# Kernel optimization log

Measured on AMD Instinct MI355X. Metric: run time of the kernel, lower is better.

The kernel has to match this reference:

```python
import jax, jax.numpy as jnp
import numpy as np
from functools import partial

T = 2048        # num tokens
H = 2048        # hidden_size
I = 1024        # intermediate_size (per TP rank)
E = 8           # num_local_experts
TOP_K = 2       # num_experts_per_tok


def setup_inputs() -> dict:
    key = jax.random.key(0)
    k1, k2, k3, k4 = jax.random.split(key, 4)
    hidden_states = jax.random.normal(k1, (T, H), dtype=jnp.float32)
    gate_w = jax.random.normal(k2, (E, H), dtype=jnp.float32) * (H ** -0.5)
    # ws: [E, 2I, H] merged w1(gate)+w3(up); w2s: [E, H, I]
    ws = jax.random.normal(k3, (E, 2 * I, H), dtype=jnp.float32) * (H ** -0.5)
    w2s = jax.random.normal(k4, (E, H, I), dtype=jnp.float32) * (I ** -0.5)
    return {"hidden_states": hidden_states, "gate_w": gate_w, "ws": ws, "w2s": w2s}


def _moe_forward(x, gate_w, ws, w2s):
    num_tokens = x.shape[0]
    # router: replicated linear -> softmax -> top-k (fused_topk semantics)
    router_logits = x @ gate_w.T                     # [T, E]
    probs = jax.nn.softmax(router_logits, axis=-1)
    topk_weights, topk_ids = jax.lax.top_k(probs, TOP_K)   # [T, K]
    if TOP_K > 1:  # renormalize (do_normalize = top_k > 1)
        topk_weights = topk_weights / jnp.sum(topk_weights, axis=-1, keepdims=True)
    # combine weights as dense [T, E] (zero where expert not selected)
    cw = jnp.zeros((num_tokens, E), dtype=x.dtype)
    cw = cw.at[jnp.arange(num_tokens)[:, None], topk_ids].add(topk_weights)
    # grouped expert GEMMs; loop over the small fixed expert set
    out = jnp.zeros_like(x)
    for e in range(E):
        gate_up = x @ ws[e].T                        # [T, 2I]
        act = jax.nn.silu(gate_up[:, :I]) * gate_up[:, I:]  # SiluAndMul
        out = out + cw[:, e:e + 1] * (act @ w2s[e].T)       # [T, H]
    return out


def reference(hidden_states, gate_w, ws, w2s):
    return _moe_forward(hidden_states, gate_w, ws, w2s)
```

## Files before the change

### kernel.cpp

```cpp
#include <hip/hip_runtime.h>
#include <hip/hip_bf16.h>
#include <stdint.h>

#define TOKS  2048
#define HID   2048
#define ITR   1024
#define NEXP  8
#define NROWS 4096

typedef __attribute__((ext_vector_type(4))) float f32x4;
typedef __attribute__((ext_vector_type(8))) __bf16 bf16x8;
typedef __attribute__((ext_vector_type(8))) unsigned short u16x8;
typedef __attribute__((ext_vector_type(4))) unsigned short u16x4;

__device__ __forceinline__ unsigned short f2bf(float f) {
    union { float f; uint32_t u; } c; c.f = f;
    return (unsigned short)((c.u + 0x7FFFu + ((c.u >> 16) & 1u)) >> 16);
}

__device__ __forceinline__ void gll16(const unsigned short* g, unsigned short* l) {
    __builtin_amdgcn_global_load_lds(
        (const __attribute__((address_space(1))) unsigned int*)g,
        (__attribute__((address_space(3))) unsigned int*)l,
        16, 0, 0);
}

__global__ __launch_bounds__(256) void prep_kernel(const float* __restrict__ ws,
                                                   const float* __restrict__ w2s,
                                                   float* __restrict__ out,
                                                   unsigned short* __restrict__ da,
                                                   unsigned short* __restrict__ db) {
    const int NA = (NEXP * 2 * ITR * HID) / 8;
    const int NB = (NEXP * HID * ITR) / 8;
    const int NO = (TOKS * HID) / 8;
    const int i0 = blockIdx.x * 256 + threadIdx.x;
    const int stride = gridDim.x * 256;
    for (int k = i0; k < NA; k += stride) {
        const f32x4* p = (const f32x4*)(ws + (size_t)k * 8);
        f32x4 a = p[0], b = p[1];
        u16x8 o;
#pragma unroll
        for (int j = 0; j < 4; ++j) { o[j] = f2bf(a[j]); o[4 + j] = f2bf(b[j]); }
        *(u16x8*)(da + (size_t)k * 8) = o;
    }
    for (int k = i0; k < NB; k += stride) {
        const f32x4* p = (const f32x4*)(w2s + (size_t)k * 8);
        f32x4 a = p[0], b = p[1];
        u16x8 o;
#pragma unroll
        for (int j = 0; j < 4; ++j) { o[j] = f2bf(a[j]); o[4 + j] = f2bf(b[j]); }
        *(u16x8*)(db + (size_t)k * 8) = o;
    }
    const f32x4 z = (f32x4){0.f, 0.f, 0.f, 0.f};
    for (int k = i0; k < NO; k += stride) {
        f32x4* q = (f32x4*)(out + (size_t)k * 8);
        q[0] = z; q[1] = z;
    }
}

__global__ __launch_bounds__(64) void router_kernel(const float* __restrict__ x,
                                                    const float* __restrict__ gw,
                                                    unsigned short* __restrict__ xb,
                                                    int* __restrict__ topk_id,
                                                    float* __restrict__ topk_w) {
    const int t = blockIdx.x;
    const int lane = threadIdx.x;
    float acc[NEXP];
#pragma unroll
    for (int e = 0; e < NEXP; ++e) acc[e] = 0.f;
    const float* xr = x + (size_t)t * HID;
    unsigned short* xbr = xb + (size_t)t * HID;
    for (int s4 = lane; s4 < HID / 4; s4 += 64) {
        const f32x4 xv = *(const f32x4*)(xr + s4 * 4);
        u16x4 o;
#pragma unroll
        for (int j = 0; j < 4; ++j) o[j] = f2bf(xv[j]);
        *(u16x4*)(xbr + s4 * 4) = o;
#pragma unroll
        for (int e = 0; e < NEXP; ++e) {
            const f32x4 gv = *(const f32x4*)(gw + e * HID + s4 * 4);
            acc[e] += xv[0] * gv[0] + xv[1] * gv[1] + xv[2] * gv[2] + xv[3] * gv[3];
        }
    }
#pragma unroll
    for (int e = 0; e < NEXP; ++e) {
        float v = acc[e];
        for (int off = 32; off > 0; off >>= 1) v += __shfl_down(v, off, 64);
        acc[e] = v;
    }
    if (lane == 0) {
        float m0 = -1e30f, m1 = -1e30f; int i0 = 0, i1 = 0;
#pragma unroll
        for (int e = 0; e < NEXP; ++e) {
            float v = acc[e];
            if (v > m0) { m1 = m0; i1 = i0; m0 = v; i0 = e; }
            else if (v > m1) { m1 = v; i1 = e; }
        }
        float w0 = 1.f / (1.f + expf(m1 - m0));
        float w1 = 1.f - w0;
        topk_id[t * 2] = i0; topk_id[t * 2 + 1] = i1;
        topk_w[t * 2] = w0;  topk_w[t * 2 + 1] = w1;
    }
}

__global__ __launch_bounds__(512) void sort_kernel(const int* __restrict__ topk_id,
                                                   const float* __restrict__ topk_w,
                                                   int* __restrict__ sorted_tok,
                                                   float* __restrict__ row_w,
                                                   int* __restrict__ offsets,
                                                   int* __restrict__ counts) {
    __shared__ int sc[512 * NEXP];
    __shared__ int base[NEXP + 1];
    const int t = threadIdx.x;
    int ids[8];
    int* myrow = &sc[t * NEXP];
#pragma unroll
    for (int e = 0; e < NEXP; ++e) myrow[e] = 0;
#pragma unroll
    for (int j = 0; j < 8; ++j) { ids[j] = topk_id[t * 8 + j]; myrow[ids[j]]++; }
    __syncthreads();
    for (int d = 1; d < 512; d <<= 1) {
        int add[NEXP];
        const bool act = (t >= d);
#pragma unroll
        for (int e = 0; e < NEXP; ++e) add[e] = act ? sc[(t - d) * NEXP + e] : 0;
        __syncthreads();
        if (act) {
#pragma unroll
            for (int e = 0; e < NEXP; ++e) sc[t * NEXP + e] += add[e];
        }
        __syncthreads();
    }
    if (t == 0) {
        int s = 0;
        for (int e = 0; e < NEXP; ++e) {
            const int tot = sc[511 * NEXP + e];
            base[e] = s; offsets[e] = s; counts[e] = tot; s += tot;
        }
        base[NEXP] = s; offsets[NEXP] = s;
    }
    __syncthreads();
    int own[NEXP];
#pragma unroll
    for (int e = 0; e < NEXP; ++e) {
        int c = 0;
#pragma unroll
        for (int j = 0; j < 8; ++j) c += (ids[j] == e) ? 1 : 0;
        own[e] = c;
    }
#pragma unroll
    for (int e = 0; e < NEXP; ++e) myrow[e] = base[e] + myrow[e] - own[e];
#pragma unroll
    for (int j = 0; j < 8; ++j) {
        const int p = t * 8 + j;
        const int pos = myrow[ids[j]]++;
        sorted_tok[pos] = p >> 1;
        row_w[pos] = topk_w[p];
    }
}

__global__ __launch_bounds__(512) void gemm1_kernel(const unsigned short* __restrict__ Wb,
                                                    const unsigned short* __restrict__ Xb,
                                                    const int* __restrict__ offsets,
                                                    const int* __restrict__ counts,
                                                    const int* __restrict__ sorted_tok,
                                                    unsigned short* __restrict__ act) {
    const int b = blockIdx.x;
    const int e = b & 7;
    const int r = b >> 3;
    const int mt = r >> 4;
    const int nt = r & 15;
    const int cnt = counts[e];
    if (mt * 128 >= cnt) return;
    const int offs = offsets[e];
    const int tid = threadIdx.x, lane = tid & 63, wid = tid >> 6;
    const int wr = wid >> 2, wc = wid & 3;

    __shared__ unsigned short sA[3][128 * 32];
    __shared__ unsigned short sB[3][128 * 32];

    const int srow = tid >> 2;
    const int swz = (((tid & 3) ^ (srow & 3))) * 8;
    int ar = mt * 128 + srow;
    if (ar >= cnt) ar = cnt - 1;
    const int tok = sorted_tok[offs + ar];
    const unsigned short* aSrc = Xb + (size_t)tok * HID + swz;
    const unsigned short* wBase = Wb + (size_t)e * (2 * ITR) * HID;
    const int wrow = (srow < 64) ? (nt * 64 + srow) : (ITR + nt * 64 + (srow - 64));
    const unsigned short* bSrc = wBase + (size_t)wrow * HID + swz;
    const int ldsOff = wid * 16 * 32;

    f32x4 accg[4], accu[4];
#pragma unroll
    for (int i = 0; i < 4; ++i) {
        accg[i] = (f32x4){0.f, 0.f, 0.f, 0.f};
        accu[i] = (f32x4){0.f, 0.f, 0.f, 0.f};
    }

#define G1_STAGE(ks) do {                                  \
        const int k0_ = (ks) * 32;                         \
        gll16(aSrc + k0_, sA[(ks) % 3] + ldsOff);          \
        gll16(bSrc + k0_, sB[(ks) % 3] + ldsOff);          \
    } while (0)

    G1_STAGE(0);
    G1_STAGE(1);

    const int fr = lane & 15, fq = lane >> 4;
    const int sfo = (fq ^ (fr & 3)) * 8;
    const int NS = HID / 32;
    for (int ks = 0; ks < NS; ++ks) {
        const int cur = ks % 3;
        if (ks == NS - 1) asm volatile("s_waitcnt vmcnt(0)" ::: "memory");
        else              asm volatile("s_waitcnt vmcnt(2)" ::: "memory");
        __builtin_amdgcn_s_barrier();
        asm volatile("" ::: "memory");
        if (ks + 2 < NS) G1_STAGE(ks + 2);
        bf16x8 af[4], bg, bu;
#pragma unroll
        for (int mi = 0; mi < 4; ++mi)
            af[mi] = *(const bf16x8*)&sA[cur][(wr * 64 + mi * 16 + fr) * 32 + sfo];
        bg = *(const bf16x8*)&sB[cur][(wc * 16 + fr) * 32 + sfo];
        bu = *(const bf16x8*)&sB[cur][(64 + wc * 16 + fr) * 32 + sfo];
        __builtin_amdgcn_s_setprio(1);
#pragma unroll
        for (int mi = 0; mi < 4; ++mi) {
            accg[mi] = __builtin_amdgcn_mfma_f32_16x16x32_bf16(af[mi], bg, accg[mi], 0, 0, 0);
            accu[mi] = __builtin_amdgcn_mfma_f32_16x16x32_bf16(af[mi], bu, accu[mi], 0, 0, 0);
        }
        __builtin_amdgcn_s_setprio(0);
        asm volatile("" ::: "memory");
    }
#undef G1_STAGE

#pragma unroll
    for (int mi = 0; mi < 4; ++mi) {
#pragma unroll
        for (int j = 0; j < 4; ++j) {
            const int gr = mt * 128 + wr * 64 + mi * 16 + fq * 4 + j;
            if (gr < cnt) {
                const float g = accg[mi][j], u = accu[mi][j];
                const float s = g / (1.f + expf(-g));
                act[(size_t)(offs + gr) * ITR + nt * 64 + wc * 16 + fr] = f2bf(s * u);
            }
        }
    }
}

__global__ __launch_bounds__(512) void gemm2_kernel(const unsigned short* __restrict__ W2b,
                                                    const unsigned short* __restrict__ actb,
                                                    const int* __restrict__ offsets,
                                                    const int* __restrict__ counts,
                                                    const int* __restrict__ sorted_tok,
                                                    const float* __restrict__ row_w,
                                                    float* __restrict__ out) {
    const int b = blockIdx.x;
    const int e = b & 7;
    const int r = b >> 3;
    const int mt = r >> 4;
    const int nt = r & 15;
    const int cnt = counts[e];
    if (mt * 128 >= cnt) return;
    const int offs = offsets[e];
    const int tid = threadIdx.x, lane = tid & 63, wid = tid >> 6;
    const int wr = wid >> 2, wc = wid & 3;

    __shared__ unsigned short sA[3][128 * 32];
    __shared__ unsigned short sB[3][128 * 32];

    const int srow = tid >> 2;
    const int swz = (((tid & 3) ^ (srow & 3))) * 8;
    int ar = mt * 128 + srow;
    if (ar >= cnt) ar = cnt - 1;
    const unsigned short* aSrc = actb + (size_t)(offs + ar) * ITR + swz;
    const unsigned short* bSrc = W2b + ((size_t)e * HID + nt * 128 + srow) * ITR + swz;
    const int ldsOff = wid * 16 * 32;

    f32x4 acc[4][2];
#pragma unroll
    for (int i = 0; i < 4; ++i)
#pragma unroll
        for (int j = 0; j < 2; ++j) acc[i][j] = (f32x4){0.f, 0.f, 0.f, 0.f};

#define G2_STAGE(ks) do {                                  \
        const int k0_ = (ks) * 32;                         \
        gll16(aSrc + k0_, sA[(ks) % 3] + ldsOff);          \
        gll16(bSrc + k0_, sB[(ks) % 3] + ldsOff);          \
    } while (0)

    G2_STAGE(0);
    G2_STAGE(1);

    const int fr = lane & 15, fq = lane >> 4;
    const int sfo = (fq ^ (fr & 3)) * 8;
    const int NS = ITR / 32;
    for (int ks = 0; ks < NS; ++ks) {
        const int cur = ks % 3;
        if (ks == NS - 1) asm volatile("s_waitcnt vmcnt(0)" ::: "memory");
        else              asm volatile("s_waitcnt vmcnt(2)" ::: "memory");
        __builtin_amdgcn_s_barrier();
        asm volatile("" ::: "memory");
        if (ks + 2 < NS) G2_STAGE(ks + 2);
        bf16x8 af[4], bfv[2];
#pragma unroll
        for (int mi = 0; mi < 4; ++mi)
            af[mi] = *(const bf16x8*)&sA[cur][(wr * 64 + mi * 16 + fr) * 32 + sfo];
#pragma unroll
        for (int ni = 0; ni < 2; ++ni)
            bfv[ni] = *(const bf16x8*)&sB[cur][(wc * 32 + ni * 16 + fr) * 32 + sfo];
        __builtin_amdgcn_s_setprio(1);
#pragma unroll
        for (int mi = 0; mi < 4; ++mi)
#pragma unroll
            for (int ni = 0; ni < 2; ++ni)
                acc[mi][ni] = __builtin_amdgcn_mfma_f32_16x16x32_bf16(af[mi], bfv[ni], acc[mi][ni], 0, 0, 0);
        __builtin_amdgcn_s_setprio(0);
        asm volatile("" ::: "memory");
    }
#undef G2_STAGE

#pragma unroll
    for (int mi = 0; mi < 4; ++mi) {
#pragma unroll
        for (int j = 0; j < 4; ++j) {
            const int gr = mt * 128 + wr * 64 + mi * 16 + fq * 4 + j;
            if (gr < cnt) {
                const int pos = offs + gr;
                const int t = sorted_tok[pos];
                const float w = row_w[pos];
#pragma unroll
                for (int ni = 0; ni < 2; ++ni) {
                    const int col = nt * 128 + wc * 32 + ni * 16 + fr;
                    atomicAdd(&out[(size_t)t * HID + col], w * acc[mi][ni][j]);
                }
            }
        }
    }
}

extern "C" void kernel_launch(void* const* d_in, const int* in_sizes, int n_in,
                              void* d_out, int out_size, void* d_ws, size_t ws_size,
                              hipStream_t stream) {
    const float* x   = (const float*)d_in[0];
    const float* gw  = (const float*)d_in[1];
    const float* ws  = (const float*)d_in[2];
    const float* w2s = (const float*)d_in[3];
    float* out = (float*)d_out;

    char* wsb = (char*)d_ws;
    int*   counts     = (int*)(wsb + 0);
    int*   offsets    = (int*)(wsb + 256);
    int*   topk_id    = (int*)(wsb + 4096);
    float* topk_w     = (float*)(wsb + 20480);
    int*   sorted_tok = (int*)(wsb + 36864);
    float* row_w      = (float*)(wsb + 53248);
    unsigned short* xb    = (unsigned short*)(wsb + (1u << 20));
    unsigned short* actb  = (unsigned short*)(wsb + 9437184);
    unsigned short* wsb16 = (unsigned short*)(wsb + 17825792);
    unsigned short* w2b   = (unsigned short*)(wsb + 84934656);

    prep_kernel<<<2048, 256, 0, stream>>>(ws, w2s, out, wsb16, w2b);
    router_kernel<<<TOKS, 64, 0, stream>>>(x, gw, xb, topk_id, topk_w);
    sort_kernel<<<1, 512, 0, stream>>>(topk_id, topk_w, sorted_tok, row_w, offsets, counts);
    gemm1_kernel<<<2048, 512, 0, stream>>>(wsb16, xb, offsets, counts, sorted_tok, actb);
    gemm2_kernel<<<2048, 512, 0, stream>>>(w2b, actb, offsets, counts, sorted_tok, row_w, out);
}
```

Measured before the change: 174.9 us.

## Fuse router into prep kernel, widen conversion loads, reorder GEMM tile indexing

The router computation moves into the weight-conversion prep kernel, run by the first wave of each of the 2048 blocks, which removes one kernel launch. The fp32-to-bf16 conversion and output zeroing now process 16 elements per thread iteration instead of 8. Both GEMMs swap the mt/nt decode of the block index so that consecutive blocks of an expert walk M tiles within a fixed N tile, which changes weight-tile reuse in cache and the ordering of early-exit blocks. The router work adds imbalance to one wave per prep block, but prep is dominated by converting about 200MB of weights.

```diff
diff --git a/kernel.cpp b/kernel.cpp
--- a/kernel.cpp
+++ b/kernel.cpp
@@ -27,79 +27,87 @@
 
 __global__ __launch_bounds__(256) void prep_kernel(const float* __restrict__ ws,
                                                    const float* __restrict__ w2s,
+                                                   const float* __restrict__ x,
+                                                   const float* __restrict__ gw,
                                                    float* __restrict__ out,
                                                    unsigned short* __restrict__ da,
-                                                   unsigned short* __restrict__ db) {
-    const int NA = (NEXP * 2 * ITR * HID) / 8;
-    const int NB = (NEXP * HID * ITR) / 8;
-    const int NO = (TOKS * HID) / 8;
-    const int i0 = blockIdx.x * 256 + threadIdx.x;
+                                                   unsigned short* __restrict__ db,
+                                                   unsigned short* __restrict__ xb,
+                                                   int* __restrict__ topk_id,
+                                                   float* __restrict__ topk_w) {
+    const int tid = threadIdx.x;
+
+    if (tid < 64) {
+        const int t = blockIdx.x;
+        const int lane = tid;
+        float acc[NEXP];
+#pragma unroll
+        for (int e = 0; e < NEXP; ++e) acc[e] = 0.f;
+        const float* xr = x + (size_t)t * HID;
+        unsigned short* xbr = xb + (size_t)t * HID;
+        for (int s4 = lane; s4 < HID / 4; s4 += 64) {
+            const f32x4 xv = *(const f32x4*)(xr + s4 * 4);
+            u16x4 o;
+#pragma unroll
+            for (int j = 0; j < 4; ++j) o[j] = f2bf(xv[j]);
+            *(u16x4*)(xbr + s4 * 4) = o;
+#pragma unroll
+            for (int e = 0; e < NEXP; ++e) {
+                const f32x4 gv = *(const f32x4*)(gw + e * HID + s4 * 4);
+                acc[e] += xv[0] * gv[0] + xv[1] * gv[1] + xv[2] * gv[2] + xv[3] * gv[3];
+            }
+        }
+#pragma unroll
+        for (int e = 0; e < NEXP; ++e) {
+            float v = acc[e];
+            for (int off = 32; off > 0; off >>= 1) v += __shfl_down(v, off, 64);
+            acc[e] = v;
+        }
+        if (lane == 0) {
+            float m0 = -1e30f, m1 = -1e30f; int i0 = 0, i1 = 0;
+#pragma unroll
+            for (int e = 0; e < NEXP; ++e) {
+                float v = acc[e];
+                if (v > m0) { m1 = m0; i1 = i0; m0 = v; i0 = e; }
+                else if (v > m1) { m1 = v; i1 = e; }
+            }
+            float w0 = 1.f / (1.f + expf(m1 - m0));
+            topk_id[t * 2] = i0; topk_id[t * 2 + 1] = i1;
+            topk_w[t * 2] = w0;  topk_w[t * 2 + 1] = 1.f - w0;
+        }
+    }
+
+    const int NA = (NEXP * 2 * ITR * HID) / 16;
+    const int NB = (NEXP * HID * ITR) / 16;
+    const int NO = (TOKS * HID) / 16;
+    const int i0 = blockIdx.x * 256 + tid;
     const int stride = gridDim.x * 256;
     for (int k = i0; k < NA; k += stride) {
-        const f32x4* p = (const f32x4*)(ws + (size_t)k * 8);
-        f32x4 a = p[0], b = p[1];
-        u16x8 o;
-#pragma unroll
-        for (int j = 0; j < 4; ++j) { o[j] = f2bf(a[j]); o[4 + j] = f2bf(b[j]); }
-        *(u16x8*)(da + (size_t)k * 8) = o;
+        const f32x4* p = (const f32x4*)(ws + (size_t)k * 16);
+        f32x4 a = p[0], b = p[1], c = p[2], d = p[3];
+        u16x8 o0, o1;
+#pragma unroll
+        for (int j = 0; j < 4; ++j) { o0[j] = f2bf(a[j]); o0[4 + j] = f2bf(b[j]); }
+#pragma unroll
+        for (int j = 0; j < 4; ++j) { o1[j] = f2bf(c[j]); o1[4 + j] = f2bf(d[j]); }
+        *(u16x8*)(da + (size_t)k * 16) = o0;
+        *(u16x8*)(da + (size_t)k * 16 + 8) = o1;
     }
     for (int k = i0; k < NB; k += stride) {
-        const f32x4* p = (const f32x4*)(w2s + (size_t)k * 8);
-        f32x4 a = p[0], b = p[1];
-        u16x8 o;
-#pragma unroll
-        for (int j = 0; j < 4; ++j) { o[j] = f2bf(a[j]); o[4 + j] = f2bf(b[j]); }
-        *(u16x8*)(db + (size_t)k * 8) = o;
+        const f32x4* p = (const f32x4*)(w2s + (size_t)k * 16);
+        f32x4 a = p[0], b = p[1], c = p[2], d = p[3];
+        u16x8 o0, o1;
+#pragma unroll
+        for (int j = 0; j < 4; ++j) { o0[j] = f2bf(a[j]); o0[4 + j] = f2bf(b[j]); }
+#pragma unroll
+        for (int j = 0; j < 4; ++j) { o1[j] = f2bf(c[j]); o1[4 + j] = f2bf(d[j]); }
+        *(u16x8*)(db + (size_t)k * 16) = o0;
+        *(u16x8*)(db + (size_t)k * 16 + 8) = o1;
     }
     const f32x4 z = (f32x4){0.f, 0.f, 0.f, 0.f};
     for (int k = i0; k < NO; k += stride) {
-        f32x4* q = (f32x4*)(out + (size_t)k * 8);
-        q[0] = z; q[1] = z;
-    }
-}
-
-__global__ __launch_bounds__(64) void router_kernel(const float* __restrict__ x,
-                                                    const float* __restrict__ gw,
-                                                    unsigned short* __restrict__ xb,
-                                                    int* __restrict__ topk_id,
-                                                    float* __restrict__ topk_w) {
-    const int t = blockIdx.x;
-    const int lane = threadIdx.x;
-    float acc[NEXP];
-#pragma unroll
-    for (int e = 0; e < NEXP; ++e) acc[e] = 0.f;
-    const float* xr = x + (size_t)t * HID;
-    unsigned short* xbr = xb + (size_t)t * HID;
-    for (int s4 = lane; s4 < HID / 4; s4 += 64) {
-        const f32x4 xv = *(const f32x4*)(xr + s4 * 4);
-        u16x4 o;
-#pragma unroll
-        for (int j = 0; j < 4; ++j) o[j] = f2bf(xv[j]);
-        *(u16x4*)(xbr + s4 * 4) = o;
-#pragma unroll
-        for (int e = 0; e < NEXP; ++e) {
-            const f32x4 gv = *(const f32x4*)(gw + e * HID + s4 * 4);
-            acc[e] += xv[0] * gv[0] + xv[1] * gv[1] + xv[2] * gv[2] + xv[3] * gv[3];
-        }
-    }
-#pragma unroll
-    for (int e = 0; e < NEXP; ++e) {
-        float v = acc[e];
-        for (int off = 32; off > 0; off >>= 1) v += __shfl_down(v, off, 64);
-        acc[e] = v;
-    }
-    if (lane == 0) {
-        float m0 = -1e30f, m1 = -1e30f; int i0 = 0, i1 = 0;
-#pragma unroll
-        for (int e = 0; e < NEXP; ++e) {
-            float v = acc[e];
-            if (v > m0) { m1 = m0; i1 = i0; m0 = v; i0 = e; }
-            else if (v > m1) { m1 = v; i1 = e; }
-        }
-        float w0 = 1.f / (1.f + expf(m1 - m0));
-        float w1 = 1.f - w0;
-        topk_id[t * 2] = i0; topk_id[t * 2 + 1] = i1;
-        topk_w[t * 2] = w0;  topk_w[t * 2 + 1] = w1;
+        f32x4* q = (f32x4*)(out + (size_t)k * 16);
+        q[0] = z; q[1] = z; q[2] = z; q[3] = z;
     }
 }
 
@@ -168,8 +176,8 @@
     const int b = blockIdx.x;
     const int e = b & 7;
     const int r = b >> 3;
-    const int mt = r >> 4;
-    const int nt = r & 15;
+    const int nt = r >> 4;
+    const int mt = r & 15;
     const int cnt = counts[e];
     if (mt * 128 >= cnt) return;
     const int offs = offsets[e];
@@ -257,8 +265,8 @@
     const int b = blockIdx.x;
     const int e = b & 7;
     const int r = b >> 3;
-    const int mt = r >> 4;
-    const int nt = r & 15;
+    const int nt = r >> 4;
+    const int mt = r & 15;
     const int cnt = counts[e];
     if (mt * 128 >= cnt) return;
     const int offs = offsets[e];
@@ -359,8 +367,7 @@
     unsigned short* wsb16 = (unsigned short*)(wsb + 17825792);
     unsigned short* w2b   = (unsigned short*)(wsb + 84934656);
 
-    prep_kernel<<<2048, 256, 0, stream>>>(ws, w2s, out, wsb16, w2b);
-    router_kernel<<<TOKS, 64, 0, stream>>>(x, gw, xb, topk_id, topk_w);
+    prep_kernel<<<2048, 256, 0, stream>>>(ws, w2s, x, gw, out, wsb16, w2b, xb, topk_id, topk_w);
     sort_kernel<<<1, 512, 0, stream>>>(topk_id, topk_w, sorted_tok, row_w, offsets, counts);
     gemm1_kernel<<<2048, 512, 0, stream>>>(wsb16, xb, offsets, counts, sorted_tok, actb);
     gemm2_kernel<<<2048, 512, 0, stream>>>(w2b, actb, offsets, counts, sorted_tok, row_w, out);
```

Measured after the change: 234.6 us. +34.2%, slower.

## Fuse fp32-to-bf16 weight conversion into GEMM loads, drop prep kernel

Applied to the files above, without the earlier changes.

Removes the separate prep pass that converted all expert weights to bf16 and zeroed the output. The GEMM kernels now stream fp32 weights straight into LDS via global_load_lds and convert to bf16 in registers before each MFMA, and the output is zeroed with hipMemsetAsync. This saves one full read-and-write pass over the weights. In exchange, B-tile global traffic and LDS footprint double, each stage issues an extra load, and per-iteration conversion ALU work is added. Weight tiles are also re-read from global memory by every M-tile block rather than once.

```diff
diff --git a/kernel.cpp b/kernel.cpp
--- a/kernel.cpp
+++ b/kernel.cpp
@@ -18,44 +18,11 @@
     return (unsigned short)((c.u + 0x7FFFu + ((c.u >> 16) & 1u)) >> 16);
 }
 
-__device__ __forceinline__ void gll16(const unsigned short* g, unsigned short* l) {
+__device__ __forceinline__ void gll16(const void* g, void* l) {
     __builtin_amdgcn_global_load_lds(
         (const __attribute__((address_space(1))) unsigned int*)g,
         (__attribute__((address_space(3))) unsigned int*)l,
         16, 0, 0);
-}
-
-__global__ __launch_bounds__(256) void prep_kernel(const float* __restrict__ ws,
-                                                   const float* __restrict__ w2s,
-                                                   float* __restrict__ out,
-                                                   unsigned short* __restrict__ da,
-                                                   unsigned short* __restrict__ db) {
-    const int NA = (NEXP * 2 * ITR * HID) / 8;
-    const int NB = (NEXP * HID * ITR) / 8;
-    const int NO = (TOKS * HID) / 8;
-    const int i0 = blockIdx.x * 256 + threadIdx.x;
-    const int stride = gridDim.x * 256;
-    for (int k = i0; k < NA; k += stride) {
-        const f32x4* p = (const f32x4*)(ws + (size_t)k * 8);
-        f32x4 a = p[0], b = p[1];
-        u16x8 o;
-#pragma unroll
-        for (int j = 0; j < 4; ++j) { o[j] = f2bf(a[j]); o[4 + j] = f2bf(b[j]); }
-        *(u16x8*)(da + (size_t)k * 8) = o;
-    }
-    for (int k = i0; k < NB; k += stride) {
-        const f32x4* p = (const f32x4*)(w2s + (size_t)k * 8);
-        f32x4 a = p[0], b = p[1];
-        u16x8 o;
-#pragma unroll
-        for (int j = 0; j < 4; ++j) { o[j] = f2bf(a[j]); o[4 + j] = f2bf(b[j]); }
-        *(u16x8*)(db + (size_t)k * 8) = o;
-    }
-    const f32x4 z = (f32x4){0.f, 0.f, 0.f, 0.f};
-    for (int k = i0; k < NO; k += stride) {
-        f32x4* q = (f32x4*)(out + (size_t)k * 8);
-        q[0] = z; q[1] = z;
-    }
 }
 
 __global__ __launch_bounds__(64) void router_kernel(const float* __restrict__ x,
@@ -97,9 +64,8 @@
             else if (v > m1) { m1 = v; i1 = e; }
         }
         float w0 = 1.f / (1.f + expf(m1 - m0));
-        float w1 = 1.f - w0;
         topk_id[t * 2] = i0; topk_id[t * 2 + 1] = i1;
-        topk_w[t * 2] = w0;  topk_w[t * 2 + 1] = w1;
+        topk_w[t * 2] = w0;  topk_w[t * 2 + 1] = 1.f - w0;
     }
 }
 
@@ -159,7 +125,7 @@
     }
 }
 
-__global__ __launch_bounds__(512) void gemm1_kernel(const unsigned short* __restrict__ Wb,
+__global__ __launch_bounds__(512) void gemm1_kernel(const float* __restrict__ W,
                                                     const unsigned short* __restrict__ Xb,
                                                     const int* __restrict__ offsets,
                                                     const int* __restrict__ counts,
@@ -177,7 +143,7 @@
     const int wr = wid >> 2, wc = wid & 3;
 
     __shared__ unsigned short sA[3][128 * 32];
-    __shared__ unsigned short sB[3][128 * 32];
+    __shared__ float sBf[3][128 * 32];
 
     const int srow = tid >> 2;
     const int swz = (((tid & 3) ^ (srow & 3))) * 8;
@@ -185,10 +151,19 @@
     if (ar >= cnt) ar = cnt - 1;
     const int tok = sorted_tok[offs + ar];
     const unsigned short* aSrc = Xb + (size_t)tok * HID + swz;
-    const unsigned short* wBase = Wb + (size_t)e * (2 * ITR) * HID;
-    const int wrow = (srow < 64) ? (nt * 64 + srow) : (ITR + nt * 64 + (srow - 64));
-    const unsigned short* bSrc = wBase + (size_t)wrow * HID + swz;
-    const int ldsOff = wid * 16 * 32;
+    const int ldsA = wid * 16 * 32;
+
+    const int l8 = lane & 7;
+    const int rr = lane >> 3;
+    const int foff = (((l8 >> 1) ^ (rr & 3)) * 8) + (l8 & 1) * 4;
+    const int R1 = wid * 16 + rr;
+    const int R2 = R1 + 8;
+    const int g1row = (R1 < 64) ? (nt * 64 + R1) : (ITR + nt * 64 + (R1 - 64));
+    const int g2row = (R2 < 64) ? (nt * 64 + R2) : (ITR + nt * 64 + (R2 - 64));
+    const float* bSrc1 = W + ((size_t)e * 2 * ITR + g1row) * HID + foff;
+    const float* bSrc2 = W + ((size_t)e * 2 * ITR + g2row) * HID + foff;
+    const int ldsB1 = (wid * 16) * 32;
+    const int ldsB2 = (wid * 16 + 8) * 32;
 
     f32x4 accg[4], accu[4];
 #pragma unroll
@@ -199,8 +174,9 @@
 
 #define G1_STAGE(ks) do {                                  \
         const int k0_ = (ks) * 32;                         \
-        gll16(aSrc + k0_, sA[(ks) % 3] + ldsOff);          \
-        gll16(bSrc + k0_, sB[(ks) % 3] + ldsOff);          \
+        gll16(aSrc + k0_, sA[(ks) % 3] + ldsA);            \
+        gll16(bSrc1 + k0_, sBf[(ks) % 3] + ldsB1);         \
+        gll16(bSrc2 + k0_, sBf[(ks) % 3] + ldsB2);         \
     } while (0)
 
     G1_STAGE(0);
@@ -208,20 +184,29 @@
 
     const int fr = lane & 15, fq = lane >> 4;
     const int sfo = (fq ^ (fr & 3)) * 8;
+    const int slot32 = fq ^ (fr & 3);
     const int NS = HID / 32;
     for (int ks = 0; ks < NS; ++ks) {
         const int cur = ks % 3;
         if (ks == NS - 1) asm volatile("s_waitcnt vmcnt(0)" ::: "memory");
-        else              asm volatile("s_waitcnt vmcnt(2)" ::: "memory");
+        else              asm volatile("s_waitcnt vmcnt(3)" ::: "memory");
         __builtin_amdgcn_s_barrier();
         asm volatile("" ::: "memory");
         if (ks + 2 < NS) G1_STAGE(ks + 2);
-        bf16x8 af[4], bg, bu;
+        bf16x8 af[4];
 #pragma unroll
         for (int mi = 0; mi < 4; ++mi)
             af[mi] = *(const bf16x8*)&sA[cur][(wr * 64 + mi * 16 + fr) * 32 + sfo];
-        bg = *(const bf16x8*)&sB[cur][(wc * 16 + fr) * 32 + sfo];
-        bu = *(const bf16x8*)&sB[cur][(64 + wc * 16 + fr) * 32 + sfo];
+        const float* pg = &sBf[cur][(wc * 16 + fr) * 32 + slot32 * 8];
+        const float* pu = &sBf[cur][(64 + wc * 16 + fr) * 32 + slot32 * 8];
+        const f32x4 g0 = *(const f32x4*)pg, g1 = *(const f32x4*)(pg + 4);
+        const f32x4 u0 = *(const f32x4*)pu, u1 = *(const f32x4*)(pu + 4);
+        bf16x8 bg, bu;
+#pragma unroll
+        for (int j = 0; j < 4; ++j) {
+            bg[j] = (__bf16)g0[j]; bg[4 + j] = (__bf16)g1[j];
+            bu[j] = (__bf16)u0[j]; bu[4 + j] = (__bf16)u1[j];
+        }
         __builtin_amdgcn_s_setprio(1);
 #pragma unroll
         for (int mi = 0; mi < 4; ++mi) {
@@ -247,7 +232,7 @@
     }
 }
 
-__global__ __launch_bounds__(512) void gemm2_kernel(const unsigned short* __restrict__ W2b,
+__global__ __launch_bounds__(512) void gemm2_kernel(const float* __restrict__ W2,
                                                     const unsigned short* __restrict__ actb,
                                                     const int* __restrict__ offsets,
                                                     const int* __restrict__ counts,
@@ -266,15 +251,24 @@
     const int wr = wid >> 2, wc = wid & 3;
 
     __shared__ unsigned short sA[3][128 * 32];
-    __shared__ unsigned short sB[3][128 * 32];
+    __shared__ float sBf[3][128 * 32];
 
     const int srow = tid >> 2;
     const int swz = (((tid & 3) ^ (srow & 3))) * 8;
     int ar = mt * 128 + srow;
     if (ar >= cnt) ar = cnt - 1;
     const unsigned short* aSrc = actb + (size_t)(offs + ar) * ITR + swz;
-    const unsigned short* bSrc = W2b + ((size_t)e * HID + nt * 128 + srow) * ITR + swz;
-    const int ldsOff = wid * 16 * 32;
+    const int ldsA = wid * 16 * 32;
+
+    const int l8 = lane & 7;
+    const int rr = lane >> 3;
+    const int foff = (((l8 >> 1) ^ (rr & 3)) * 8) + (l8 & 1) * 4;
+    const int R1 = wid * 16 + rr;
+    const int R2 = R1 + 8;
+    const float* bSrc1 = W2 + ((size_t)e * HID + nt * 128 + R1) * ITR + foff;
+    const float* bSrc2 = W2 + ((size_t)e * HID + nt * 128 + R2) * ITR + foff;
+    const int ldsB1 = (wid * 16) * 32;
+    const int ldsB2 = (wid * 16 + 8) * 32;
 
     f32x4 acc[4][2];
 #pragma unroll
@@ -284,8 +278,9 @@
 
 #define G2_STAGE(ks) do {                                  \
         const int k0_ = (ks) * 32;                         \
-        gll16(aSrc + k0_, sA[(ks) % 3] + ldsOff);          \
-        gll16(bSrc + k0_, sB[(ks) % 3] + ldsOff);          \
+        gll16(aSrc + k0_, sA[(ks) % 3] + ldsA);            \
+        gll16(bSrc1 + k0_, sBf[(ks) % 3] + ldsB1);         \
+        gll16(bSrc2 + k0_, sBf[(ks) % 3] + ldsB2);         \
     } while (0)
 
     G2_STAGE(0);
@@ -293,21 +288,27 @@
 
     const int fr = lane & 15, fq = lane >> 4;
     const int sfo = (fq ^ (fr & 3)) * 8;
+    const int slot32 = fq ^ (fr & 3);
     const int NS = ITR / 32;
     for (int ks = 0; ks < NS; ++ks) {
         const int cur = ks % 3;
         if (ks == NS - 1) asm volatile("s_waitcnt vmcnt(0)" ::: "memory");
-        else              asm volatile("s_waitcnt vmcnt(2)" ::: "memory");
+        else              asm volatile("s_waitcnt vmcnt(3)" ::: "memory");
         __builtin_amdgcn_s_barrier();
         asm volatile("" ::: "memory");
         if (ks + 2 < NS) G2_STAGE(ks + 2);
-        bf16x8 af[4], bfv[2];
+        bf16x8 af[4];
 #pragma unroll
         for (int mi = 0; mi < 4; ++mi)
             af[mi] = *(const bf16x8*)&sA[cur][(wr * 64 + mi * 16 + fr) * 32 + sfo];
-#pragma unroll
-        for (int ni = 0; ni < 2; ++ni)
-            bfv[ni] = *(const bf16x8*)&sB[cur][(wc * 32 + ni * 16 + fr) * 32 + sfo];
+        bf16x8 bfv[2];
+#pragma unroll
+        for (int ni = 0; ni < 2; ++ni) {
+            const float* pb = &sBf[cur][(wc * 32 + ni * 16 + fr) * 32 + slot32 * 8];
+            const f32x4 v0 = *(const f32x4*)pb, v1 = *(const f32x4*)(pb + 4);
+#pragma unroll
+            for (int j = 0; j < 4; ++j) { bfv[ni][j] = (__bf16)v0[j]; bfv[ni][4 + j] = (__bf16)v1[j]; }
+        }
         __builtin_amdgcn_s_setprio(1);
 #pragma unroll
         for (int mi = 0; mi < 4; ++mi)
@@ -354,14 +355,12 @@
     float* topk_w     = (float*)(wsb + 20480);
     int*   sorted_tok = (int*)(wsb + 36864);
     float* row_w      = (float*)(wsb + 53248);
-    unsigned short* xb    = (unsigned short*)(wsb + (1u << 20));
-    unsigned short* actb  = (unsigned short*)(wsb + 9437184);
-    unsigned short* wsb16 = (unsigned short*)(wsb + 17825792);
-    unsigned short* w2b   = (unsigned short*)(wsb + 84934656);
-
-    prep_kernel<<<2048, 256, 0, stream>>>(ws, w2s, out, wsb16, w2b);
+    unsigned short* xb   = (unsigned short*)(wsb + (1u << 20));
+    unsigned short* actb = (unsigned short*)(wsb + 9437184);
+
+    hipMemsetAsync(out, 0, (size_t)out_size * sizeof(float), stream);
     router_kernel<<<TOKS, 64, 0, stream>>>(x, gw, xb, topk_id, topk_w);
     sort_kernel<<<1, 512, 0, stream>>>(topk_id, topk_w, sorted_tok, row_w, offsets, counts);
-    gemm1_kernel<<<2048, 512, 0, stream>>>(wsb16, xb, offsets, counts, sorted_tok, actb);
-    gemm2_kernel<<<2048, 512, 0, stream>>>(w2b, actb, offsets, counts, sorted_tok, row_w, out);
-}
+    gemm1_kernel<<<2048, 512, 0, stream>>>(ws, xb, offsets, counts, sorted_tok, actb);
+    gemm2_kernel<<<2048, 512, 0, stream>>>(w2s, actb, offsets, counts, sorted_tok, row_w, out);
+}
```

New measurement: 207.4 us. +18.6%, slower.
